# Optimization experiments

Measured on AMD Instinct MI355X. Metric: run time of the kernel, lower is better.

The kernel has to match this reference:

```python
import jax, jax.numpy as jnp
import numpy as np

N = 100000   # nodes
E = 1600000  # edges (avg degree 16)
D = 128      # input_dim == output_dim (residual requires equality)
BN_EPS = 1e-5


def setup_inputs() -> dict:
    key = jax.random.key(0)
    ks = jax.random.split(key, 8)
    X = jax.random.normal(ks[0], (N, D), dtype=jnp.float32)
    E_X = jax.random.normal(ks[1], (E, D), dtype=jnp.float32)
    snorm_n = jax.random.uniform(ks[2], (N, 1), dtype=jnp.float32)
    snorm_e = jax.random.uniform(ks[3], (E, 1), dtype=jnp.float32)
    src = jax.random.randint(ks[4], (E,), 0, N, dtype=jnp.int32)
    dst = jax.random.randint(ks[5], (E,), 0, N, dtype=jnp.int32)
    # Linear A and B parameters (torch nn.Linear: y = x @ W.T + b)
    scale = 1.0 / np.sqrt(D)
    A_w = jax.random.uniform(ks[6], (D, D), dtype=jnp.float32, minval=-scale, maxval=scale)
    B_w = jax.random.uniform(ks[7], (D, D), dtype=jnp.float32, minval=-scale, maxval=scale)
    A_b = jnp.zeros((D,), jnp.float32)
    B_b = jnp.zeros((D,), jnp.float32)
    # BatchNorm1d affine params (training mode -> batch stats)
    gamma = jnp.ones((D,), jnp.float32)
    beta = jnp.zeros((D,), jnp.float32)
    return {"X": X, "E_X": E_X, "snorm_n": snorm_n, "snorm_e": snorm_e,
            "src": src, "dst": dst, "A_w": A_w, "A_b": A_b,
            "B_w": B_w, "B_b": B_b, "gamma": gamma, "beta": beta}


def reference(X, E_X, snorm_n, snorm_e, src, dst, A_w, A_b, B_w, B_b, gamma, beta):
    AX = X @ A_w.T + A_b                       # [N, D]
    BX = X @ B_w.T + B_b                       # [N, D]
    # message: gather BX at edge sources; reduce: sum into destinations
    msgs = BX[src]                             # [E, D] irregular gather
    agg = jax.ops.segment_sum(msgs, dst, num_segments=N)  # [N, D]
    # DGL custom reduce only fires for nodes with in-degree > 0;
    # zero-in-degree nodes keep H = X
    indeg = jax.ops.segment_sum(jnp.ones((E,), X.dtype), dst, num_segments=N)
    H = jnp.where(indeg[:, None] > 0, AX + agg, X)
    H = H * snorm_n
    # BatchNorm1d (training mode: biased batch statistics)
    mean = jnp.mean(H, axis=0)
    var = jnp.mean((H - mean) ** 2, axis=0)
    H = (H - mean) * jax.lax.rsqrt(var + BN_EPS) * gamma + beta
    H = jax.nn.relu(H)
    H = X + H                                  # residual
    return (H, E_X)
```

## Files before the change

kernel.cpp:

```cpp
#include <hip/hip_runtime.h>

#define D 128
#define NNODES 100000
#define NEDGES 1600000
#define BN_EPS 1e-5f
#define NB_STATS 2048
#define NBLK_P 391

#define OFF_AX     12800000
#define OFF_BX16   25600000
#define OFF_ESRC   32000000
#define OFF_ORDER  33600000
#define OFF_INDEG  35200000
#define OFF_ROWS   35300000
#define OFF_LEXC   35500000
#define OFF_BPART  35700000
#define OFF_BSCAN  35701000
#define OFF_PSUM   35800000
#define OFF_PSQ    36100000
#define OFF_SCALE  36400000
#define OFF_SHIFT  36400128

static __device__ __forceinline__ unsigned short f2bf(float f) {
    unsigned int u = __float_as_uint(f);
    u = (u + 0x7FFF + ((u >> 16) & 1)) >> 16;
    return (unsigned short)u;
}
static __device__ __forceinline__ float bf_lo(unsigned v) {
    return __uint_as_float(v << 16);
}
static __device__ __forceinline__ float bf_hi(unsigned v) {
    return __uint_as_float(v & 0xFFFF0000u);
}

__global__ __launch_bounds__(256, 2) void gemm2_kernel(
    const float* __restrict__ X,
    const float* __restrict__ Aw, const float* __restrict__ Ab,
    const float* __restrict__ Bw, const float* __restrict__ Bb,
    float* __restrict__ AX, unsigned short* __restrict__ BX16)
{
    const bool isB = (blockIdx.x & 1);
    const float* __restrict__ W    = isB ? Bw : Aw;
    const float* __restrict__ bias = isB ? Bb : Ab;

    __shared__ float Ws[D * 132];
    const float4* W4 = (const float4*)W;
    for (int i = threadIdx.x; i < D * D / 4; i += 256) {
        int d  = i >> 5;
        int k4 = i & 31;
        float4 w = W4[i];
        *(float4*)&Ws[d * 132 + 4 * k4] = w;
    }
    __syncthreads();

    const int rg = threadIdx.x >> 5;
    const int cg = threadIdx.x & 31;

    float b[4];
#pragma unroll
    for (int j = 0; j < 4; ++j) b[j] = bias[cg + 32 * j];

    const int ntiles = NNODES / 32;
    for (int t = (blockIdx.x >> 1); t < ntiles; t += (gridDim.x >> 1)) {
        const int row0 = t * 32 + rg * 4;
        float acc[4][4];
#pragma unroll
        for (int r = 0; r < 4; ++r)
#pragma unroll
            for (int j = 0; j < 4; ++j) acc[r][j] = b[j];

        const float* xbase = X + (size_t)row0 * D;
#pragma unroll 4
        for (int k = 0; k < D; k += 4) {
            float4 xr[4];
#pragma unroll
            for (int r = 0; r < 4; ++r)
                xr[r] = *(const float4*)&xbase[r * D + k];
            float4 wv[4];
#pragma unroll
            for (int j = 0; j < 4; ++j)
                wv[j] = *(const float4*)&Ws[(cg + 32 * j) * 132 + k];
#pragma unroll
            for (int r = 0; r < 4; ++r)
#pragma unroll
                for (int j = 0; j < 4; ++j)
                    acc[r][j] += xr[r].x * wv[j].x + xr[r].y * wv[j].y +
                                 xr[r].z * wv[j].z + xr[r].w * wv[j].w;
        }
        if (isB) {
#pragma unroll
            for (int r = 0; r < 4; ++r) {
                unsigned short* yrow = BX16 + (size_t)(row0 + r) * D;
#pragma unroll
                for (int j = 0; j < 4; ++j)
                    yrow[cg + 32 * j] = f2bf(acc[r][j]);
            }
        } else {
#pragma unroll
            for (int r = 0; r < 4; ++r) {
                float* yrow = AX + (size_t)(row0 + r) * D;
#pragma unroll
                for (int j = 0; j < 4; ++j) yrow[cg + 32 * j] = acc[r][j];
            }
        }
    }
}

__global__ __launch_bounds__(256) void hist_kernel(
    const int* __restrict__ dst, int* __restrict__ indeg,
    int* __restrict__ order)
{
    for (int e = blockIdx.x * 256 + threadIdx.x; e < NEDGES;
         e += gridDim.x * 256)
        order[e] = atomicAdd(&indeg[dst[e]], 1);
}

__global__ __launch_bounds__(256) void scan1_kernel(
    const int* __restrict__ indeg, int* __restrict__ lexc,
    int* __restrict__ bpart)
{
    __shared__ int ls[256];
    const int i = blockIdx.x * 256 + threadIdx.x;
    const int v = (i < NNODES) ? indeg[i] : 0;
    ls[threadIdx.x] = v;
    __syncthreads();
    for (int off = 1; off < 256; off <<= 1) {
        int u = (threadIdx.x >= off) ? ls[threadIdx.x - off] : 0;
        __syncthreads();
        ls[threadIdx.x] += u;
        __syncthreads();
    }
    if (i < NNODES) lexc[i] = ls[threadIdx.x] - v;
    if (threadIdx.x == 255) bpart[blockIdx.x] = ls[255];
}

__global__ __launch_bounds__(512) void scan2_kernel(
    const int* __restrict__ bpart, int* __restrict__ bscan,
    int* __restrict__ rows)
{
    __shared__ int ls[512];
    const int t = threadIdx.x;
    const int v = (t < NBLK_P) ? bpart[t] : 0;
    ls[t] = v;
    __syncthreads();
    for (int off = 1; off < 512; off <<= 1) {
        int u = (t >= off) ? ls[t - off] : 0;
        __syncthreads();
        ls[t] += u;
        __syncthreads();
    }
    if (t < NBLK_P) bscan[t] = ls[t] - v;
    if (t == 0) rows[NNODES] = NEDGES;
}

__global__ __launch_bounds__(256) void scan3_kernel(
    const int* __restrict__ lexc, const int* __restrict__ bscan,
    int* __restrict__ rows)
{
    const int i = blockIdx.x * 256 + threadIdx.x;
    if (i < NNODES) rows[i] = bscan[blockIdx.x] + lexc[i];
}

__global__ __launch_bounds__(256) void fill_kernel(
    const int* __restrict__ src, const int* __restrict__ dst,
    const int* __restrict__ rows, const int* __restrict__ order,
    int* __restrict__ esrc)
{
    for (int e = blockIdx.x * 256 + threadIdx.x; e < NEDGES;
         e += gridDim.x * 256) {
        esrc[rows[dst[e]] + order[e]] = src[e];
    }
}

__global__ __launch_bounds__(256, 4) void agg_kernel(
    const float* __restrict__ AX, const unsigned* __restrict__ BX32,
    const float* __restrict__ X, const float* __restrict__ snorm,
    const int* __restrict__ rows, const int* __restrict__ esrc,
    float* __restrict__ Hpre, float* __restrict__ psum,
    float* __restrict__ psq)
{
    const int w    = threadIdx.x >> 6;
    const int lane = threadIdx.x & 63;
    const int c0   = lane * 2;
    float ps0 = 0.f, ps1 = 0.f, q0 = 0.f, q1 = 0.f;

    for (int i = blockIdx.x * 4 + w; i < NNODES; i += gridDim.x * 4) {
        const int rs = rows[i];
        const int re = rows[i + 1];
        float ax, ay;
        if (re > rs) {
            float2 a0 = *(const float2*)&AX[(size_t)i * D + c0];
            ax = a0.x; ay = a0.y;
            int e = rs;
            for (; e + 4 <= re; e += 4) {
                const int s0 = esrc[e + 0], s1 = esrc[e + 1];
                const int s2 = esrc[e + 2], s3 = esrc[e + 3];
                const unsigned v0 = BX32[s0 * 64 + lane];
                const unsigned v1 = BX32[s1 * 64 + lane];
                const unsigned v2 = BX32[s2 * 64 + lane];
                const unsigned v3 = BX32[s3 * 64 + lane];
                ax += bf_lo(v0) + bf_lo(v1) + bf_lo(v2) + bf_lo(v3);
                ay += bf_hi(v0) + bf_hi(v1) + bf_hi(v2) + bf_hi(v3);
            }
            for (; e < re; ++e) {
                const unsigned v = BX32[esrc[e] * 64 + lane];
                ax += bf_lo(v);
                ay += bf_hi(v);
            }
        } else {
            float2 x0 = *(const float2*)&X[(size_t)i * D + c0];
            ax = x0.x; ay = x0.y;
        }
        const float sn = snorm[i];
        ax *= sn; ay *= sn;
        *(float2*)&Hpre[(size_t)i * D + c0] = make_float2(ax, ay);
        ps0 += ax; ps1 += ay;
        q0  += ax * ax; q1 += ay * ay;
    }

    __shared__ float sp[4][D], sq[4][D];
    sp[w][c0] = ps0; sp[w][c0 + 1] = ps1;
    sq[w][c0] = q0;  sq[w][c0 + 1] = q1;
    __syncthreads();
    if (threadIdx.x < D) {
        const int c = threadIdx.x;
        psum[blockIdx.x * D + c] = sp[0][c] + sp[1][c] + sp[2][c] + sp[3][c];
        psq [blockIdx.x * D + c] = sq[0][c] + sq[1][c] + sq[2][c] + sq[3][c];
    }
}

__global__ __launch_bounds__(1024) void bnstats_kernel(
    const float* __restrict__ psum, const float* __restrict__ psq,
    const float* __restrict__ gamma, const float* __restrict__ beta,
    float* __restrict__ scale, float* __restrict__ shift)
{
    const int c = threadIdx.x & 127;
    const int g = threadIdx.x >> 7;
    float s = 0.f, q = 0.f;
    for (int b = g; b < NB_STATS; b += 8) {
        s += psum[b * D + c];
        q += psq [b * D + c];
    }
    __shared__ float ls[8][D], lq[8][D];
    ls[g][c] = s;
    lq[g][c] = q;
    __syncthreads();
    if (threadIdx.x < D) {
        float S = 0.f, Q = 0.f;
#pragma unroll
        for (int g2 = 0; g2 < 8; ++g2) { S += ls[g2][c]; Q += lq[g2][c]; }
        const float inv_n = 1.0f / (float)NNODES;
        float mean = S * inv_n;
        float var  = Q * inv_n - mean * mean;
        float sc   = rsqrtf(var + BN_EPS) * gamma[c];
        scale[c] = sc;
        shift[c] = beta[c] - mean * sc;
    }
}

__global__ __launch_bounds__(256) void final_kernel(
    const float* __restrict__ Hpre, const float* __restrict__ X,
    const float* __restrict__ scale, const float* __restrict__ shift,
    float* __restrict__ out)
{
    const int total = NNODES * D / 4;
    for (int i = blockIdx.x * 256 + threadIdx.x; i < total;
         i += gridDim.x * 256) {
        float4 h = ((const float4*)Hpre)[i];
        float4 x = ((const float4*)X)[i];
        int d0 = (i * 4) & 127;
        float4 r;
        r.x = x.x + fmaxf(0.f, h.x * scale[d0 + 0] + shift[d0 + 0]);
        r.y = x.y + fmaxf(0.f, h.y * scale[d0 + 1] + shift[d0 + 1]);
        r.z = x.z + fmaxf(0.f, h.z * scale[d0 + 2] + shift[d0 + 2]);
        r.w = x.w + fmaxf(0.f, h.w * scale[d0 + 3] + shift[d0 + 3]);
        ((float4*)out)[i] = r;
    }
}

extern "C" void kernel_launch(void* const* d_in, const int* in_sizes, int n_in,
                              void* d_out, int out_size, void* d_ws, size_t ws_size,
                              hipStream_t stream)
{
    const float* X       = (const float*)d_in[0];
    const float* E_X     = (const float*)d_in[1];
    const float* snorm_n = (const float*)d_in[2];
    const int*   src     = (const int*)d_in[4];
    const int*   dst     = (const int*)d_in[5];
    const float* A_w     = (const float*)d_in[6];
    const float* A_b     = (const float*)d_in[7];
    const float* B_w     = (const float*)d_in[8];
    const float* B_b     = (const float*)d_in[9];
    const float* gamma   = (const float*)d_in[10];
    const float* beta    = (const float*)d_in[11];

    float* out = (float*)d_out;

    float*          AX    = out + OFF_AX;
    unsigned short* BX16  = (unsigned short*)(out + OFF_BX16);
    int*            esrc  = (int*)(out + OFF_ESRC);
    int*            order = (int*)(out + OFF_ORDER);
    int*            indeg = (int*)(out + OFF_INDEG);
    int*            rows  = (int*)(out + OFF_ROWS);
    int*            lexc  = (int*)(out + OFF_LEXC);
    int*            bpart = (int*)(out + OFF_BPART);
    int*            bscan = (int*)(out + OFF_BSCAN);
    float*          psum  = out + OFF_PSUM;
    float*          psq   = out + OFF_PSQ;
    float*          scale = out + OFF_SCALE;
    float*          shift = out + OFF_SHIFT;

    hipMemsetAsync(indeg, 0, NNODES * sizeof(int), stream);

    gemm2_kernel<<<512, 256, 0, stream>>>(X, A_w, A_b, B_w, B_b, AX, BX16);
    hist_kernel<<<2048, 256, 0, stream>>>(dst, indeg, order);
    scan1_kernel<<<NBLK_P, 256, 0, stream>>>(indeg, lexc, bpart);
    scan2_kernel<<<1, 512, 0, stream>>>(bpart, bscan, rows);
    scan3_kernel<<<NBLK_P, 256, 0, stream>>>(lexc, bscan, rows);
    fill_kernel<<<2048, 256, 0, stream>>>(src, dst, rows, order, esrc);
    agg_kernel<<<NB_STATS, 256, 0, stream>>>(AX, (const unsigned*)BX16, X,
                                             snorm_n, rows, esrc,
                                             out, psum, psq);
    bnstats_kernel<<<1, 1024, 0, stream>>>(psum, psq, gamma, beta, scale, shift);
    final_kernel<<<2048, 256, 0, stream>>>(out, X, scale, shift, out);

    hipMemcpyAsync(out + (size_t)NNODES * D, E_X,
                   (size_t)NEDGES * D * sizeof(float),
                   hipMemcpyDeviceToDevice, stream);
}
```

Baseline: 744.8 us.

## Overlap E_X passthrough copy with compute kernels via extra copy blocks

Splits the large E_X device-to-device copy into chunks and appends extra blocks to each compute kernel that copy one chunk, so the copy bandwidth overlaps with the latency-bound graph kernels instead of running as a separate memcpy at the end. Scratch buffers move into the workspace when it is large enough, instead of living in the E_X region of the output. This frees that region so it can be written early. The copy blocks compete for bandwidth and CU slots with the main work, and the fallback path keeps the old behaviour.

```diff
diff --git a/kernel.cpp b/kernel.cpp
--- a/kernel.cpp
+++ b/kernel.cpp
@@ -7,19 +7,36 @@
 #define NB_STATS 2048
 #define NBLK_P 391
 
-#define OFF_AX     12800000
-#define OFF_BX16   25600000
-#define OFF_ESRC   32000000
-#define OFF_ORDER  33600000
-#define OFF_INDEG  35200000
-#define OFF_ROWS   35300000
-#define OFF_LEXC   35500000
-#define OFF_BPART  35700000
-#define OFF_BSCAN  35701000
-#define OFF_PSUM   35800000
-#define OFF_PSQ    36100000
-#define OFF_SCALE  36400000
-#define OFF_SHIFT  36400128
+#define OFF_AX     0
+#define OFF_BX16   12800000
+#define OFF_ESRC   19200000
+#define OFF_ORDER  20800000
+#define OFF_INDEG  22400000
+#define OFF_ROWS   22510000
+#define OFF_LEXC   22620000
+#define OFF_BPART  22730000
+#define OFF_BSCAN  22731000
+#define OFF_PSUM   22740000
+#define OFF_PSQ    23010000
+#define OFF_SCALE  23280000
+#define OFF_SHIFT  23280128
+#define WS_NEED_BYTES 93200000ull
+
+#define MAIN_GEMM 512
+#define MAIN_EDGE 2048
+#define MAIN_AGG  2048
+#define MAIN_FIN  2048
+
+#define C_GEMM0   0L
+#define C_GEMM1   16000000L
+#define C_HIST1   21000000L
+#define C_SCAN1   22000000L
+#define C_SCAN2   23000000L
+#define C_SCAN3   24000000L
+#define C_FILL1   29000000L
+#define C_AGG1    46000000L
+#define C_BN1     48000000L
+#define C_FIN1    51200000L
 
 static __device__ __forceinline__ unsigned short f2bf(float f) {
     unsigned int u = __float_as_uint(f);
@@ -33,12 +50,28 @@
     return __uint_as_float(v & 0xFFFF0000u);
 }
 
+static __device__ __forceinline__ void ex_copy(
+    const float4* __restrict__ s, float4* __restrict__ d,
+    long c0, long c1, int cb, int ncb)
+{
+    for (long i = c0 + (long)cb * blockDim.x + threadIdx.x; i < c1;
+         i += (long)ncb * blockDim.x)
+        d[i] = s[i];
+}
+
 __global__ __launch_bounds__(256, 2) void gemm2_kernel(
     const float* __restrict__ X,
     const float* __restrict__ Aw, const float* __restrict__ Ab,
     const float* __restrict__ Bw, const float* __restrict__ Bb,
-    float* __restrict__ AX, unsigned short* __restrict__ BX16)
-{
+    float* __restrict__ AX, unsigned short* __restrict__ BX16,
+    const float4* __restrict__ exs, float4* __restrict__ exd,
+    long c0, long c1)
+{
+    if (blockIdx.x >= MAIN_GEMM) {
+        ex_copy(exs, exd, c0, c1, blockIdx.x - MAIN_GEMM,
+                gridDim.x - MAIN_GEMM);
+        return;
+    }
     const bool isB = (blockIdx.x & 1);
     const float* __restrict__ W    = isB ? Bw : Aw;
     const float* __restrict__ bias = isB ? Bb : Ab;
@@ -61,7 +94,7 @@
     for (int j = 0; j < 4; ++j) b[j] = bias[cg + 32 * j];
 
     const int ntiles = NNODES / 32;
-    for (int t = (blockIdx.x >> 1); t < ntiles; t += (gridDim.x >> 1)) {
+    for (int t = (blockIdx.x >> 1); t < ntiles; t += (MAIN_GEMM >> 1)) {
         const int row0 = t * 32 + rg * 4;
         float acc[4][4];
 #pragma unroll
@@ -108,17 +141,30 @@
 
 __global__ __launch_bounds__(256) void hist_kernel(
     const int* __restrict__ dst, int* __restrict__ indeg,
-    int* __restrict__ order)
-{
+    int* __restrict__ order,
+    const float4* __restrict__ exs, float4* __restrict__ exd,
+    long c0, long c1)
+{
+    if (blockIdx.x >= MAIN_EDGE) {
+        ex_copy(exs, exd, c0, c1, blockIdx.x - MAIN_EDGE,
+                gridDim.x - MAIN_EDGE);
+        return;
+    }
     for (int e = blockIdx.x * 256 + threadIdx.x; e < NEDGES;
-         e += gridDim.x * 256)
+         e += MAIN_EDGE * 256)
         order[e] = atomicAdd(&indeg[dst[e]], 1);
 }
 
 __global__ __launch_bounds__(256) void scan1_kernel(
     const int* __restrict__ indeg, int* __restrict__ lexc,
-    int* __restrict__ bpart)
-{
+    int* __restrict__ bpart,
+    const float4* __restrict__ exs, float4* __restrict__ exd,
+    long c0, long c1)
+{
+    if (blockIdx.x >= NBLK_P) {
+        ex_copy(exs, exd, c0, c1, blockIdx.x - NBLK_P, gridDim.x - NBLK_P);
+        return;
+    }
     __shared__ int ls[256];
     const int i = blockIdx.x * 256 + threadIdx.x;
     const int v = (i < NNODES) ? indeg[i] : 0;
@@ -136,8 +182,14 @@
 
 __global__ __launch_bounds__(512) void scan2_kernel(
     const int* __restrict__ bpart, int* __restrict__ bscan,
-    int* __restrict__ rows)
-{
+    int* __restrict__ rows,
+    const float4* __restrict__ exs, float4* __restrict__ exd,
+    long c0, long c1)
+{
+    if (blockIdx.x >= 1) {
+        ex_copy(exs, exd, c0, c1, blockIdx.x - 1, gridDim.x - 1);
+        return;
+    }
     __shared__ int ls[512];
     const int t = threadIdx.x;
     const int v = (t < NBLK_P) ? bpart[t] : 0;
@@ -155,8 +207,14 @@
 
 __global__ __launch_bounds__(256) void scan3_kernel(
     const int* __restrict__ lexc, const int* __restrict__ bscan,
-    int* __restrict__ rows)
-{
+    int* __restrict__ rows,
+    const float4* __restrict__ exs, float4* __restrict__ exd,
+    long c0, long c1)
+{
+    if (blockIdx.x >= NBLK_P) {
+        ex_copy(exs, exd, c0, c1, blockIdx.x - NBLK_P, gridDim.x - NBLK_P);
+        return;
+    }
     const int i = blockIdx.x * 256 + threadIdx.x;
     if (i < NNODES) rows[i] = bscan[blockIdx.x] + lexc[i];
 }
@@ -164,10 +222,17 @@
 __global__ __launch_bounds__(256) void fill_kernel(
     const int* __restrict__ src, const int* __restrict__ dst,
     const int* __restrict__ rows, const int* __restrict__ order,
-    int* __restrict__ esrc)
-{
+    int* __restrict__ esrc,
+    const float4* __restrict__ exs, float4* __restrict__ exd,
+    long c0, long c1)
+{
+    if (blockIdx.x >= MAIN_EDGE) {
+        ex_copy(exs, exd, c0, c1, blockIdx.x - MAIN_EDGE,
+                gridDim.x - MAIN_EDGE);
+        return;
+    }
     for (int e = blockIdx.x * 256 + threadIdx.x; e < NEDGES;
-         e += gridDim.x * 256) {
+         e += MAIN_EDGE * 256) {
         esrc[rows[dst[e]] + order[e]] = src[e];
     }
 }
@@ -177,19 +242,26 @@
     const float* __restrict__ X, const float* __restrict__ snorm,
     const int* __restrict__ rows, const int* __restrict__ esrc,
     float* __restrict__ Hpre, float* __restrict__ psum,
-    float* __restrict__ psq)
-{
+    float* __restrict__ psq,
+    const float4* __restrict__ exs, float4* __restrict__ exd,
+    long c0, long c1)
+{
+    if (blockIdx.x >= MAIN_AGG) {
+        ex_copy(exs, exd, c0, c1, blockIdx.x - MAIN_AGG,
+                gridDim.x - MAIN_AGG);
+        return;
+    }
     const int w    = threadIdx.x >> 6;
     const int lane = threadIdx.x & 63;
-    const int c0   = lane * 2;
+    const int cc0  = lane * 2;
     float ps0 = 0.f, ps1 = 0.f, q0 = 0.f, q1 = 0.f;
 
-    for (int i = blockIdx.x * 4 + w; i < NNODES; i += gridDim.x * 4) {
+    for (int i = blockIdx.x * 4 + w; i < NNODES; i += MAIN_AGG * 4) {
         const int rs = rows[i];
         const int re = rows[i + 1];
         float ax, ay;
         if (re > rs) {
-            float2 a0 = *(const float2*)&AX[(size_t)i * D + c0];
+            float2 a0 = *(const float2*)&AX[(size_t)i * D + cc0];
             ax = a0.x; ay = a0.y;
             int e = rs;
             for (; e + 4 <= re; e += 4) {
@@ -208,19 +280,19 @@
                 ay += bf_hi(v);
             }
         } else {
-            float2 x0 = *(const float2*)&X[(size_t)i * D + c0];
+            float2 x0 = *(const float2*)&X[(size_t)i * D + cc0];
             ax = x0.x; ay = x0.y;
         }
         const float sn = snorm[i];
         ax *= sn; ay *= sn;
-        *(float2*)&Hpre[(size_t)i * D + c0] = make_float2(ax, ay);
+        *(float2*)&Hpre[(size_t)i * D + cc0] = make_float2(ax, ay);
         ps0 += ax; ps1 += ay;
         q0  += ax * ax; q1 += ay * ay;
     }
 
     __shared__ float sp[4][D], sq[4][D];
-    sp[w][c0] = ps0; sp[w][c0 + 1] = ps1;
-    sq[w][c0] = q0;  sq[w][c0 + 1] = q1;
+    sp[w][cc0] = ps0; sp[w][cc0 + 1] = ps1;
+    sq[w][cc0] = q0;  sq[w][cc0 + 1] = q1;
     __syncthreads();
     if (threadIdx.x < D) {
         const int c = threadIdx.x;
@@ -232,8 +304,14 @@
 __global__ __launch_bounds__(1024) void bnstats_kernel(
     const float* __restrict__ psum, const float* __restrict__ psq,
     const float* __restrict__ gamma, const float* __restrict__ beta,
-    float* __restrict__ scale, float* __restrict__ shift)
-{
+    float* __restrict__ scale, float* __restrict__ shift,
+    const float4* __restrict__ exs, float4* __restrict__ exd,
+    long c0, long c1)
+{
+    if (blockIdx.x >= 1) {
+        ex_copy(exs, exd, c0, c1, blockIdx.x - 1, gridDim.x - 1);
+        return;
+    }
     const int c = threadIdx.x & 127;
     const int g = threadIdx.x >> 7;
     float s = 0.f, q = 0.f;
@@ -261,11 +339,18 @@
 __global__ __launch_bounds__(256) void final_kernel(
     const float* __restrict__ Hpre, const float* __restrict__ X,
     const float* __restrict__ scale, const float* __restrict__ shift,
-    float* __restrict__ out)
-{
+    float* __restrict__ out,
+    const float4* __restrict__ exs, float4* __restrict__ exd,
+    long c0, long c1)
+{
+    if (blockIdx.x >= MAIN_FIN) {
+        ex_copy(exs, exd, c0, c1, blockIdx.x - MAIN_FIN,
+                gridDim.x - MAIN_FIN);
+        return;
+    }
     const int total = NNODES * D / 4;
     for (int i = blockIdx.x * 256 + threadIdx.x; i < total;
-         i += gridDim.x * 256) {
+         i += MAIN_FIN * 256) {
         float4 h = ((const float4*)Hpre)[i];
         float4 x = ((const float4*)X)[i];
         int d0 = (i * 4) & 127;
@@ -295,36 +380,69 @@
     const float* beta    = (const float*)d_in[11];
 
     float* out = (float*)d_out;
-
-    float*          AX    = out + OFF_AX;
-    unsigned short* BX16  = (unsigned short*)(out + OFF_BX16);
-    int*            esrc  = (int*)(out + OFF_ESRC);
-    int*            order = (int*)(out + OFF_ORDER);
-    int*            indeg = (int*)(out + OFF_INDEG);
-    int*            rows  = (int*)(out + OFF_ROWS);
-    int*            lexc  = (int*)(out + OFF_LEXC);
-    int*            bpart = (int*)(out + OFF_BPART);
-    int*            bscan = (int*)(out + OFF_BSCAN);
-    float*          psum  = out + OFF_PSUM;
-    float*          psq   = out + OFF_PSQ;
-    float*          scale = out + OFF_SCALE;
-    float*          shift = out + OFF_SHIFT;
+    const bool use_ws = (ws_size >= WS_NEED_BYTES);
+    float* sb = use_ws ? (float*)d_ws : (out + (size_t)NNODES * D);
+
+    float*          AX    = sb + OFF_AX;
+    unsigned short* BX16  = (unsigned short*)(sb + OFF_BX16);
+    int*            esrc  = (int*)(sb + OFF_ESRC);
+    int*            order = (int*)(sb + OFF_ORDER);
+    int*            indeg = (int*)(sb + OFF_INDEG);
+    int*            rows  = (int*)(sb + OFF_ROWS);
+    int*            lexc  = (int*)(sb + OFF_LEXC);
+    int*            bpart = (int*)(sb + OFF_BPART);
+    int*            bscan = (int*)(sb + OFF_BSCAN);
+    float*          psum  = sb + OFF_PSUM;
+    float*          psq   = sb + OFF_PSQ;
+    float*          scale = sb + OFF_SCALE;
+    float*          shift = sb + OFF_SHIFT;
+
+    const float4* exs = (const float4*)E_X;
+    float4*       exd = (float4*)(out + (size_t)NNODES * D);
 
     hipMemsetAsync(indeg, 0, NNODES * sizeof(int), stream);
 
-    gemm2_kernel<<<512, 256, 0, stream>>>(X, A_w, A_b, B_w, B_b, AX, BX16);
-    hist_kernel<<<2048, 256, 0, stream>>>(dst, indeg, order);
-    scan1_kernel<<<NBLK_P, 256, 0, stream>>>(indeg, lexc, bpart);
-    scan2_kernel<<<1, 512, 0, stream>>>(bpart, bscan, rows);
-    scan3_kernel<<<NBLK_P, 256, 0, stream>>>(lexc, bscan, rows);
-    fill_kernel<<<2048, 256, 0, stream>>>(src, dst, rows, order, esrc);
-    agg_kernel<<<NB_STATS, 256, 0, stream>>>(AX, (const unsigned*)BX16, X,
-                                             snorm_n, rows, esrc,
-                                             out, psum, psq);
-    bnstats_kernel<<<1, 1024, 0, stream>>>(psum, psq, gamma, beta, scale, shift);
-    final_kernel<<<2048, 256, 0, stream>>>(out, X, scale, shift, out);
-
-    hipMemcpyAsync(out + (size_t)NNODES * D, E_X,
-                   (size_t)NEDGES * D * sizeof(float),
-                   hipMemcpyDeviceToDevice, stream);
-}
+    if (use_ws) {
+        gemm2_kernel<<<MAIN_GEMM + 1024, 256, 0, stream>>>(
+            X, A_w, A_b, B_w, B_b, AX, BX16, exs, exd, C_GEMM0, C_GEMM1);
+        hist_kernel<<<MAIN_EDGE + 512, 256, 0, stream>>>(
+            dst, indeg, order, exs, exd, C_GEMM1, C_HIST1);
+        scan1_kernel<<<NBLK_P + 256, 256, 0, stream>>>(
+            indeg, lexc, bpart, exs, exd, C_HIST1, C_SCAN1);
+        scan2_kernel<<<1 + 256, 512, 0, stream>>>(
+            bpart, bscan, rows, exs, exd, C_SCAN1, C_SCAN2);
+        scan3_kernel<<<NBLK_P + 256, 256, 0, stream>>>(
+            lexc, bscan, rows, exs, exd, C_SCAN2, C_SCAN3);
+        fill_kernel<<<MAIN_EDGE + 512, 256, 0, stream>>>(
+            src, dst, rows, order, esrc, exs, exd, C_SCAN3, C_FILL1);
+        agg_kernel<<<MAIN_AGG + 1024, 256, 0, stream>>>(
+            AX, (const unsigned*)BX16, X, snorm_n, rows, esrc,
+            out, psum, psq, exs, exd, C_FILL1, C_AGG1);
+        bnstats_kernel<<<1 + 256, 1024, 0, stream>>>(
+            psum, psq, gamma, beta, scale, shift, exs, exd, C_AGG1, C_BN1);
+        final_kernel<<<MAIN_FIN + 256, 256, 0, stream>>>(
+            out, X, scale, shift, out, exs, exd, C_BN1, C_FIN1);
+    } else {
+        gemm2_kernel<<<MAIN_GEMM, 256, 0, stream>>>(
+            X, A_w, A_b, B_w, B_b, AX, BX16, exs, exd, 0, 0);
+        hist_kernel<<<MAIN_EDGE, 256, 0, stream>>>(
+            dst, indeg, order, exs, exd, 0, 0);
+        scan1_kernel<<<NBLK_P, 256, 0, stream>>>(
+            indeg, lexc, bpart, exs, exd, 0, 0);
+        scan2_kernel<<<1, 512, 0, stream>>>(
+            bpart, bscan, rows, exs, exd, 0, 0);
+        scan3_kernel<<<NBLK_P, 256, 0, stream>>>(
+            lexc, bscan, rows, exs, exd, 0, 0);
+        fill_kernel<<<MAIN_EDGE, 256, 0, stream>>>(
+            src, dst, rows, order, esrc, exs, exd, 0, 0);
+        agg_kernel<<<MAIN_AGG, 256, 0, stream>>>(
+            AX, (const unsigned*)BX16, X, snorm_n, rows, esrc,
+            out, psum, psq, exs, exd, 0, 0);
+        bnstats_kernel<<<1, 1024, 0, stream>>>(
+            psum, psq, gamma, beta, scale, shift, exs, exd, 0, 0);
+        final_kernel<<<MAIN_FIN, 256, 0, stream>>>(
+            out, X, scale, shift, out, exs, exd, 0, 0);
+        hipMemcpyAsync(exd, exs, (size_t)NEDGES * D * sizeof(float),
+                       hipMemcpyDeviceToDevice, stream);
+    }
+}
```

Measured after the change: 849.8 us. +14.1%, slower.

## Overlap E_X output copy with gemm, histogram and fill kernels via workspace

Applied to the files above, without the earlier changes.

Moves intermediate buffers from the output tail into the workspace when it is large enough. This frees the E_X region of the output so chunks of the edge-feature copy can be performed inside the GEMM, histogram and fill kernels, with only the remainder copied by memcpy. The intent is to hide copy bandwidth behind latency- and atomic-bound phases. It also raises agg_kernel's occupancy hint, at the risk of register pressure and of slowing the compute kernels through bandwidth contention.

```diff
diff --git a/kernel.cpp b/kernel.cpp
--- a/kernel.cpp
+++ b/kernel.cpp
@@ -7,19 +7,35 @@
 #define NB_STATS 2048
 #define NBLK_P 391
 
-#define OFF_AX     12800000
-#define OFF_BX16   25600000
-#define OFF_ESRC   32000000
-#define OFF_ORDER  33600000
-#define OFF_INDEG  35200000
-#define OFF_ROWS   35300000
-#define OFF_LEXC   35500000
-#define OFF_BPART  35700000
-#define OFF_BSCAN  35701000
-#define OFF_PSUM   35800000
-#define OFF_PSQ    36100000
-#define OFF_SCALE  36400000
-#define OFF_SHIFT  36400128
+#define OFF_AX     0
+#define OFF_BX16   12800000
+#define OFF_ESRC   19200000
+#define OFF_ORDER  20800000
+#define OFF_INDEG  22400000
+#define OFF_ROWS   22510000
+#define OFF_LEXC   22620000
+#define OFF_BPART  22730000
+#define OFF_BSCAN  22731000
+#define OFF_PSUM   22740000
+#define OFF_PSQ    23010000
+#define OFF_SCALE  23280000
+#define OFF_SHIFT  23280128
+#define WS_NEED_BYTES 93200000ull
+
+#define MAIN_GEMM 512
+#define MAIN_EDGE 2048
+#define MAIN_AGG  2048
+#define MAIN_FIN  2048
+
+#define GEMM_BSZ   24576L
+#define GEMM_TOTAL (512L * GEMM_BSZ)
+#define HIST_BSZ   3072L
+#define HIST_START GEMM_TOTAL
+#define HIST_TOTAL (2048L * HIST_BSZ)
+#define FILL_START (HIST_START + HIST_TOTAL)
+#define FILL_TOTAL (2048L * HIST_BSZ)
+#define TAIL_START (FILL_START + FILL_TOTAL)
+#define C_TOTAL    51200000L
 
 static __device__ __forceinline__ unsigned short f2bf(float f) {
     unsigned int u = __float_as_uint(f);
@@ -37,11 +53,16 @@
     const float* __restrict__ X,
     const float* __restrict__ Aw, const float* __restrict__ Ab,
     const float* __restrict__ Bw, const float* __restrict__ Bb,
-    float* __restrict__ AX, unsigned short* __restrict__ BX16)
+    float* __restrict__ AX, unsigned short* __restrict__ BX16,
+    const float4* __restrict__ exs, float4* __restrict__ exd,
+    long bsz)
 {
     const bool isB = (blockIdx.x & 1);
     const float* __restrict__ W    = isB ? Bw : Aw;
     const float* __restrict__ bias = isB ? Bb : Ab;
+
+    long cur  = (long)blockIdx.x * bsz + threadIdx.x;
+    const long bend = (long)blockIdx.x * bsz + bsz;
 
     __shared__ float Ws[D * 132];
     const float4* W4 = (const float4*)W;
@@ -61,7 +82,7 @@
     for (int j = 0; j < 4; ++j) b[j] = bias[cg + 32 * j];
 
     const int ntiles = NNODES / 32;
-    for (int t = (blockIdx.x >> 1); t < ntiles; t += (gridDim.x >> 1)) {
+    for (int t = (blockIdx.x >> 1); t < ntiles; t += (MAIN_GEMM >> 1)) {
         const int row0 = t * 32 + rg * 4;
         float acc[4][4];
 #pragma unroll
@@ -103,16 +124,35 @@
                 for (int j = 0; j < 4; ++j) yrow[cg + 32 * j] = acc[r][j];
             }
         }
+#pragma unroll
+        for (int j = 0; j < 8; ++j) {
+            long idx = cur + j * 256;
+            if (idx < bend) exd[idx] = exs[idx];
+        }
+        cur += 2048;
     }
 }
 
 __global__ __launch_bounds__(256) void hist_kernel(
     const int* __restrict__ dst, int* __restrict__ indeg,
-    int* __restrict__ order)
-{
-    for (int e = blockIdx.x * 256 + threadIdx.x; e < NEDGES;
-         e += gridDim.x * 256)
-        order[e] = atomicAdd(&indeg[dst[e]], 1);
+    int* __restrict__ order,
+    const float4* __restrict__ exs, float4* __restrict__ exd,
+    long cstart, long cb)
+{
+    long cur  = cstart + (long)blockIdx.x * cb + threadIdx.x;
+    const long bend = cstart + (long)blockIdx.x * cb + cb;
+    int e = blockIdx.x * 256 + threadIdx.x;
+#pragma unroll 1
+    for (int it = 0; it < 4; ++it) {
+        if (e < NEDGES) order[e] = atomicAdd(&indeg[dst[e]], 1);
+#pragma unroll
+        for (int j = 0; j < 4; ++j) {
+            long idx = cur + j * 256;
+            if (idx < bend) exd[idx] = exs[idx];
+        }
+        cur += 1024;
+        e   += MAIN_EDGE * 256;
+    }
 }
 
 __global__ __launch_bounds__(256) void scan1_kernel(
@@ -164,15 +204,27 @@
 __global__ __launch_bounds__(256) void fill_kernel(
     const int* __restrict__ src, const int* __restrict__ dst,
     const int* __restrict__ rows, const int* __restrict__ order,
-    int* __restrict__ esrc)
-{
-    for (int e = blockIdx.x * 256 + threadIdx.x; e < NEDGES;
-         e += gridDim.x * 256) {
-        esrc[rows[dst[e]] + order[e]] = src[e];
-    }
-}
-
-__global__ __launch_bounds__(256, 4) void agg_kernel(
+    int* __restrict__ esrc,
+    const float4* __restrict__ exs, float4* __restrict__ exd,
+    long cstart, long cb)
+{
+    long cur  = cstart + (long)blockIdx.x * cb + threadIdx.x;
+    const long bend = cstart + (long)blockIdx.x * cb + cb;
+    int e = blockIdx.x * 256 + threadIdx.x;
+#pragma unroll 1
+    for (int it = 0; it < 4; ++it) {
+        if (e < NEDGES) esrc[rows[dst[e]] + order[e]] = src[e];
+#pragma unroll
+        for (int j = 0; j < 4; ++j) {
+            long idx = cur + j * 256;
+            if (idx < bend) exd[idx] = exs[idx];
+        }
+        cur += 1024;
+        e   += MAIN_EDGE * 256;
+    }
+}
+
+__global__ __launch_bounds__(256, 8) void agg_kernel(
     const float* __restrict__ AX, const unsigned* __restrict__ BX32,
     const float* __restrict__ X, const float* __restrict__ snorm,
     const int* __restrict__ rows, const int* __restrict__ esrc,
@@ -184,7 +236,7 @@
     const int c0   = lane * 2;
     float ps0 = 0.f, ps1 = 0.f, q0 = 0.f, q1 = 0.f;
 
-    for (int i = blockIdx.x * 4 + w; i < NNODES; i += gridDim.x * 4) {
+    for (int i = blockIdx.x * 4 + w; i < NNODES; i += MAIN_AGG * 4) {
         const int rs = rows[i];
         const int re = rows[i + 1];
         float ax, ay;
@@ -265,7 +317,7 @@
 {
     const int total = NNODES * D / 4;
     for (int i = blockIdx.x * 256 + threadIdx.x; i < total;
-         i += gridDim.x * 256) {
+         i += MAIN_FIN * 256) {
         float4 h = ((const float4*)Hpre)[i];
         float4 x = ((const float4*)X)[i];
         int d0 = (i * 4) & 127;
@@ -295,36 +347,48 @@
     const float* beta    = (const float*)d_in[11];
 
     float* out = (float*)d_out;
-
-    float*          AX    = out + OFF_AX;
-    unsigned short* BX16  = (unsigned short*)(out + OFF_BX16);
-    int*            esrc  = (int*)(out + OFF_ESRC);
-    int*            order = (int*)(out + OFF_ORDER);
-    int*            indeg = (int*)(out + OFF_INDEG);
-    int*            rows  = (int*)(out + OFF_ROWS);
-    int*            lexc  = (int*)(out + OFF_LEXC);
-    int*            bpart = (int*)(out + OFF_BPART);
-    int*            bscan = (int*)(out + OFF_BSCAN);
-    float*          psum  = out + OFF_PSUM;
-    float*          psq   = out + OFF_PSQ;
-    float*          scale = out + OFF_SCALE;
-    float*          shift = out + OFF_SHIFT;
+    const bool use_ws = (ws_size >= WS_NEED_BYTES);
+    float* sb = use_ws ? (float*)d_ws : (out + (size_t)NNODES * D);
+
+    float*          AX    = sb + OFF_AX;
+    unsigned short* BX16  = (unsigned short*)(sb + OFF_BX16);
+    int*            esrc  = (int*)(sb + OFF_ESRC);
+    int*            order = (int*)(sb + OFF_ORDER);
+    int*            indeg = (int*)(sb + OFF_INDEG);
+    int*            rows  = (int*)(sb + OFF_ROWS);
+    int*            lexc  = (int*)(sb + OFF_LEXC);
+    int*            bpart = (int*)(sb + OFF_BPART);
+    int*            bscan = (int*)(sb + OFF_BSCAN);
+    float*          psum  = sb + OFF_PSUM;
+    float*          psq   = sb + OFF_PSQ;
+    float*          scale = sb + OFF_SCALE;
+    float*          shift = sb + OFF_SHIFT;
+
+    const float4* exs = (const float4*)E_X;
+    float4*       exd = (float4*)(out + (size_t)NNODES * D);
+
+    const long gemm_bsz  = use_ws ? GEMM_BSZ : 0;
+    const long edge_cb   = use_ws ? HIST_BSZ : 0;
+    const long tail_from = use_ws ? TAIL_START : 0;
 
     hipMemsetAsync(indeg, 0, NNODES * sizeof(int), stream);
 
-    gemm2_kernel<<<512, 256, 0, stream>>>(X, A_w, A_b, B_w, B_b, AX, BX16);
-    hist_kernel<<<2048, 256, 0, stream>>>(dst, indeg, order);
+    gemm2_kernel<<<MAIN_GEMM, 256, 0, stream>>>(
+        X, A_w, A_b, B_w, B_b, AX, BX16, exs, exd, gemm_bsz);
+    hist_kernel<<<MAIN_EDGE, 256, 0, stream>>>(
+        dst, indeg, order, exs, exd, HIST_START, edge_cb);
     scan1_kernel<<<NBLK_P, 256, 0, stream>>>(indeg, lexc, bpart);
     scan2_kernel<<<1, 512, 0, stream>>>(bpart, bscan, rows);
     scan3_kernel<<<NBLK_P, 256, 0, stream>>>(lexc, bscan, rows);
-    fill_kernel<<<2048, 256, 0, stream>>>(src, dst, rows, order, esrc);
-    agg_kernel<<<NB_STATS, 256, 0, stream>>>(AX, (const unsigned*)BX16, X,
-                                             snorm_n, rows, esrc,
-                                             out, psum, psq);
-    bnstats_kernel<<<1, 1024, 0, stream>>>(psum, psq, gamma, beta, scale, shift);
-    final_kernel<<<2048, 256, 0, stream>>>(out, X, scale, shift, out);
-
-    hipMemcpyAsync(out + (size_t)NNODES * D, E_X,
-                   (size_t)NEDGES * D * sizeof(float),
+    fill_kernel<<<MAIN_EDGE, 256, 0, stream>>>(
+        src, dst, rows, order, esrc, exs, exd, FILL_START, edge_cb);
+    agg_kernel<<<MAIN_AGG, 256, 0, stream>>>(
+        AX, (const unsigned*)BX16, X, snorm_n, rows, esrc, out, psum, psq);
+    bnstats_kernel<<<1, 1024, 0, stream>>>(psum, psq, gamma, beta,
+                                           scale, shift);
+    final_kernel<<<MAIN_FIN, 256, 0, stream>>>(out, X, scale, shift, out);
+
+    hipMemcpyAsync(exd + tail_from, exs + tail_from,
+                   (size_t)(C_TOTAL - tail_from) * sizeof(float4),
                    hipMemcpyDeviceToDevice, stream);
 }
```

Result: no change. 748.8 us (+0.5%).
